# Performance work log

Hardware: AMD Instinct MI355X
Metric: run time of the kernel (lower is better)

Reference implementation:

```python
import jax, jax.numpy as jnp
from jax import lax
import numpy as np

V, B, E, H, T = 32000, 32, 64, 256, 128
START = 0


def setup_inputs() -> dict:
    key = jax.random.key(0)
    ks = jax.random.split(key, 17)
    s = 0.1  # keep logits in a sane range
    inp = {
        "input_x": jax.random.randint(ks[0], (B, T), 0, V, dtype=jnp.int32),
        "emb": jax.random.normal(ks[1], (V, E), jnp.float32) * s,
        "Wi": jax.random.normal(ks[2], (E, H), jnp.float32) * s,
        "Ui": jax.random.normal(ks[3], (H, H), jnp.float32) * s,
        "bi": jax.random.normal(ks[4], (H,), jnp.float32) * s,
        "Wf": jax.random.normal(ks[5], (E, H), jnp.float32) * s,
        "Uf": jax.random.normal(ks[6], (H, H), jnp.float32) * s,
        "bf": jax.random.normal(ks[7], (H,), jnp.float32) * s,
        "Wog": jax.random.normal(ks[8], (E, H), jnp.float32) * s,
        "Uog": jax.random.normal(ks[9], (H, H), jnp.float32) * s,
        "bog": jax.random.normal(ks[10], (H,), jnp.float32) * s,
        "Wc": jax.random.normal(ks[11], (E, H), jnp.float32) * s,
        "Uc": jax.random.normal(ks[12], (H, H), jnp.float32) * s,
        "bc": jax.random.normal(ks[13], (H,), jnp.float32) * s,
        "Wo": jax.random.normal(ks[14], (H, V), jnp.float32) * s,
        "bo": jax.random.normal(ks[15], (V,), jnp.float32) * s,
        "start_token": START,
    }
    return inp


def reference(input_x, emb, Wi, Ui, bi, Wf, Uf, bf, Wog, Uog, bog,
              Wc, Uc, bc, Wo, bo, start_token):
    b, t = input_x.shape
    h_dim = Ui.shape[0]
    # teacher-forcing inputs: [start_emb, emb(x_0..x_{T-2})], time-major [T,B,E]
    x0 = emb[jnp.full((b,), start_token, dtype=jnp.int32)]  # [B,E]
    emb_x = jnp.transpose(emb[input_x], (1, 0, 2))          # [T,B,E]
    xs = jnp.concatenate([x0[None], emb_x[:-1]], axis=0)    # [T,B,E]

    def step(carry, x):
        h, c = carry
        i = jax.nn.sigmoid(x @ Wi + h @ Ui + bi)
        f = jax.nn.sigmoid(x @ Wf + h @ Uf + bf)
        o = jax.nn.sigmoid(x @ Wog + h @ Uog + bog)
        c_bar = jnp.tanh(x @ Wc + h @ Uc + bc)
        c = f * c + i * c_bar
        h = o * jnp.tanh(c)
        logits = h @ Wo + bo                                # [B,V]
        return (h, c), jax.nn.log_softmax(logits, axis=-1)

    h0 = jnp.zeros((b, h_dim), jnp.float32)
    _, logp = lax.scan(step, (h0, h0), xs)                  # [T,B,V]
    logp = jnp.transpose(logp, (1, 0, 2))                   # [B,T,V]
    # -sum over all tokens of log p(target); equals one_hot * log(softmax) sum
    tgt_logp = jnp.take_along_axis(logp, input_x[..., None].astype(jnp.int32), axis=-1)[..., 0]
    return -jnp.sum(tgt_logp)
```

## Files before the change

### kernel.cpp

```cpp
#include <hip/hip_runtime.h>
#include <hip/hip_bf16.h>
#include <math.h>

#define V 32000
#define B 32
#define E 64
#define H 256
#define T 128
#define NROW (B*T)
#define NC 128
#define NVB (V/NC)

typedef __attribute__((ext_vector_type(8))) short bf16x8;
typedef __attribute__((ext_vector_type(4))) float f32x4;
typedef __attribute__((ext_vector_type(8))) unsigned short u16x8;

#define OFF_XS   0
#define OFF_XW   (OFF_XS + NROW*E)
#define OFF_HB   (OFF_XW + NROW*4*H)
#define OFF_PS   (OFF_HB + NROW*H/2)
#define OFF_TL   (OFF_PS + NVB*NROW)
#define OFF_U8   (OFF_TL + NROW)
#define OFF_SC   (OFF_U8 + H*H)
#define OFF_TGT  (OFF_SC + 16)

static __device__ __forceinline__ unsigned short f2bf(float f) {
    union { float f; unsigned int u; } x; x.f = f;
    unsigned int r = x.u + 0x7fffu + ((x.u >> 16) & 1u);
    return (unsigned short)(r >> 16);
}
static __device__ __forceinline__ float bf2f(unsigned short u) {
    union { unsigned int u; float f; } x; x.u = ((unsigned int)u) << 16; return x.f;
}
static __device__ __forceinline__ float sigmoidf_(float x) { return 1.f / (1.f + __expf(-x)); }
static __device__ __forceinline__ float tanhf_(float x)    { return 2.f / (1.f + __expf(-2.f * x)) - 1.f; }

#if defined(__has_builtin)
#if __has_builtin(__builtin_amdgcn_sdot4)
#define HAVE_SDOT4 1
#endif
#if __has_builtin(__builtin_amdgcn_global_load_lds)
#define HAVE_GLL 1
#endif
#endif
static __device__ __forceinline__ int dot4i8(unsigned int a, unsigned int b, int c) {
#ifdef HAVE_SDOT4
    return __builtin_amdgcn_sdot4((int)a, (int)b, c, false);
#else
    c += (int)(char)(a)       * (int)(char)(b);
    c += (int)(char)(a >> 8)  * (int)(char)(b >> 8);
    c += (int)(char)(a >> 16) * (int)(char)(b >> 16);
    c += (int)(char)(a >> 24) * (int)(char)(b >> 24);
    return c;
#endif
}
static __device__ __forceinline__ void stage16(const char* g, char* l, int lane) {
#ifdef HAVE_GLL
    __builtin_amdgcn_global_load_lds(
        (const __attribute__((address_space(1))) void*)g,
        (__attribute__((address_space(3))) void*)l, 16, 0, 0);
    (void)lane;
#else
    *(uint4*)(l + lane * 16) = *(const uint4*)g;
#endif
}

__global__ void lstm_embed(const int* __restrict__ x, const float* __restrict__ emb,
                           const int* __restrict__ start, float* __restrict__ xs,
                           float* __restrict__ out, int* __restrict__ tgtrow) {
    int idx = blockIdx.x * 256 + threadIdx.x;
    if (idx == 0) out[0] = 0.f;
    if (idx < NROW) tgtrow[idx] = x[(idx & 31) * T + (idx >> 5)];
    if (idx >= T * B * E) return;
    int t   = idx / (B * E);
    int rem = idx - t * (B * E);
    int b   = rem >> 6;
    int e   = rem & 63;
    int tok = (t == 0) ? start[0] : x[b * T + (t - 1)];
    xs[idx] = emb[tok * E + e];
}

__global__ __launch_bounds__(256) void lstm_xw(
        const float* __restrict__ xs, unsigned short* __restrict__ xwq,
        const float* __restrict__ Wi, const float* __restrict__ Wf,
        const float* __restrict__ Wog, const float* __restrict__ Wc,
        const float* __restrict__ bi, const float* __restrict__ bf,
        const float* __restrict__ bog, const float* __restrict__ bc) {
    __shared__ float xsl[32][65];
    const int t = blockIdx.x, tid = threadIdx.x;
    for (int i = tid; i < 32 * 64; i += 256) {
        int b = i >> 6, e = i & 63;
        xsl[b][e] = xs[(size_t)(t * 32 + b) * 64 + e];
    }
    __syncthreads();
    const int b = tid & 31, jg = tid >> 5;
    for (int jj = 0; jj < 32; ++jj) {
        const int j = jg * 32 + jj;
        float a0 = bi[j], a1 = bf[j], a2 = bog[j], a3 = bc[j];
        #pragma unroll 8
        for (int e = 0; e < E; ++e) {
            float xe = xsl[b][e];
            a0 += xe * Wi [e * H + j];
            a1 += xe * Wf [e * H + j];
            a2 += xe * Wog[e * H + j];
            a3 += xe * Wc [e * H + j];
        }
        ushort4 v;
        v.x = f2bf(a0); v.y = f2bf(a1); v.z = f2bf(a2); v.w = f2bf(a3);
        *(ushort4*)(xwq + ((size_t)(t * 32 + b) * 256 + j) * 4) = v;
    }
}

__global__ __launch_bounds__(256) void lstm_umax(
        const float* __restrict__ Ui, const float* __restrict__ Uf,
        const float* __restrict__ Uog, const float* __restrict__ Uc,
        float* __restrict__ sc) {
    const int g = blockIdx.x;
    const float* U = (g == 0) ? Ui : (g == 1) ? Uf : (g == 2) ? Uog : Uc;
    float m = 0.f;
    for (int i = threadIdx.x; i < H * H; i += 256) m = fmaxf(m, fabsf(U[i]));
    __shared__ float red[256];
    red[threadIdx.x] = m;
    __syncthreads();
    for (int off = 128; off > 0; off >>= 1) {
        if (threadIdx.x < off) red[threadIdx.x] = fmaxf(red[threadIdx.x], red[threadIdx.x + off]);
        __syncthreads();
    }
    if (threadIdx.x == 0) sc[g] = fmaxf(red[0], 1e-20f);
}

__global__ __launch_bounds__(256) void lstm_uq8(
        const float* __restrict__ Ui, const float* __restrict__ Uf,
        const float* __restrict__ Uog, const float* __restrict__ Uc,
        const float* __restrict__ sc, unsigned int* __restrict__ UQ8) {
    const int idx = blockIdx.x * 256 + threadIdx.x;
    const int k4 = idx >> 8, j = idx & 255;
    float inv[4] = { 127.f / sc[0], 127.f / sc[1], 127.f / sc[2], 127.f / sc[3] };
    const float* Ug[4] = { Ui, Uf, Uog, Uc };
    uint4 out;
    unsigned int* op = (unsigned int*)&out;
    #pragma unroll
    for (int g = 0; g < 4; ++g) {
        unsigned int w = 0;
        #pragma unroll
        for (int kk = 0; kk < 4; ++kk) {
            float v = Ug[g][(size_t)(k4 * 4 + kk) * H + j];
            int q = __float2int_rn(v * inv[g]);
            q = q > 127 ? 127 : (q < -127 ? -127 : q);
            w |= ((unsigned int)(q & 255)) << (kk * 8);
        }
        op[g] = w;
    }
    *(uint4*)(UQ8 + (size_t)idx * 4) = out;
}

__global__ __launch_bounds__(1024) void lstm_recur_i8(
        const unsigned short* __restrict__ xwq, const uint4* __restrict__ UQ8,
        const float* __restrict__ sc, unsigned short* __restrict__ hb) {
    __shared__ unsigned int hq8[2][64];
    __shared__ int4 red[4][256];
    const int b = blockIdx.x, tid = threadIdx.x;
    const int j = tid & 255, q = tid >> 8;
    const float f0 = sc[0] * (1.f / 16129.f), f1 = sc[1] * (1.f / 16129.f);
    const float f2 = sc[2] * (1.f / 16129.f), f3 = sc[3] * (1.f / 16129.f);
    float c_ = 0.f;

    for (int t = 0; t < T; ++t) {
        if (t > 0) {
            const uint4* up = UQ8 + (size_t)(q * 16) * 256 + j;
            const unsigned int* hrow = hq8[t & 1] + q * 16;
            int a0 = 0, a1 = 0, a2 = 0, a3 = 0;
            #pragma unroll
            for (int m = 0; m < 16; ++m) {
                uint4 u = up[(size_t)m * 256];
                unsigned int hv = hrow[m];
                a0 = dot4i8(u.x, hv, a0);
                a1 = dot4i8(u.y, hv, a1);
                a2 = dot4i8(u.z, hv, a2);
                a3 = dot4i8(u.w, hv, a3);
            }
            red[q][j] = make_int4(a0, a1, a2, a3);
        }
        __syncthreads();
        if (tid < 256) {
            ushort4 xw = *(const ushort4*)(xwq + ((size_t)(t * 32 + b) * 256 + j) * 4);
            float pi = bf2f(xw.x), pf = bf2f(xw.y), po = bf2f(xw.z), pc = bf2f(xw.w);
            if (t > 0) {
                int4 r0 = red[0][j], r1 = red[1][j], r2 = red[2][j], r3 = red[3][j];
                pi += (float)(r0.x + r1.x + r2.x + r3.x) * f0;
                pf += (float)(r0.y + r1.y + r2.y + r3.y) * f1;
                po += (float)(r0.z + r1.z + r2.z + r3.z) * f2;
                pc += (float)(r0.w + r1.w + r2.w + r3.w) * f3;
            }
            c_ = sigmoidf_(pf) * c_ + sigmoidf_(pi) * tanhf_(pc);
            float h = sigmoidf_(po) * tanhf_(c_);
            hb[(size_t)(t * B + b) * H + j] = f2bf(h);
            ((char*)hq8[(t + 1) & 1])[j] = (char)__float2int_rn(h * 127.f);
        }
        __syncthreads();
    }
}

__global__ __launch_bounds__(256) void lstm_wot(const float* __restrict__ Wo,
                                                unsigned short* __restrict__ WoT) {
    __shared__ unsigned short tle[64][65];
    const int n0 = blockIdx.x * 64, k0 = blockIdx.y * 64;
    const int tid = threadIdx.x;
    for (int i = tid; i < 64 * 64; i += 256) {
        int kk = i >> 6, nn = i & 63;
        tle[kk][nn] = f2bf(Wo[(size_t)(k0 + kk) * V + n0 + nn]);
    }
    __syncthreads();
    for (int c = tid; c < 512; c += 256) {
        int nn = c >> 3, kc = c & 7;
        u16x8 v;
        #pragma unroll
        for (int e = 0; e < 8; ++e) v[e] = tle[kc * 8 + e][nn];
        *(u16x8*)(WoT + (size_t)(n0 + nn) * H + k0 + kc * 8) = v;
    }
}

__global__ __launch_bounds__(1024, 4) void lstm_logits_mfma(
        const unsigned short* __restrict__ hb, const unsigned short* __restrict__ WoT,
        const float* __restrict__ bo, const int* __restrict__ tgtrow,
        float* __restrict__ ps, float* __restrict__ tl) {
    __shared__ char ab0[65536];
    __shared__ char ab1[65536];
    __shared__ float s_red[4][132];
    const int tid = threadIdx.x, lane = tid & 63, wid = tid >> 6;
    const int wr = wid >> 2, wc = wid & 3;
    const int lr = lane & 15, lg = lane >> 4;
    const int swz = lr & 7;
    const int vb = blockIdx.x * NC;

    #define STAGE_TILE(dst_, srcbase_) { _Pragma("unroll") \
        for (int i_ = 0; i_ < 4; ++i_) { \
            int chunk_ = (wid * 4 + i_) * 64 + lane; \
            int row_ = chunk_ >> 5, c16_ = chunk_ & 31; \
            int srcc_ = c16_ ^ (row_ & 7); \
            stage16((const char*)(srcbase_) + row_ * 512 + srcc_ * 16, \
                    (dst_) + (wid * 4 + i_) * 1024, lane); \
        } }

    STAGE_TILE(ab0, (const char*)(WoT + (size_t)vb * H));
    __syncthreads();
    bf16x8 Bf[2][8];
    {
        const char* bBase = ab0 + (wc * 32 + lr) * 512;
        #pragma unroll
        for (int nf = 0; nf < 2; ++nf)
            #pragma unroll
            for (int ks = 0; ks < 8; ++ks)
                Bf[nf][ks] = *(const bf16x8*)(bBase + nf * 16 * 512 + (((ks * 4 + lg) ^ swz) << 4));
    }
    float bocol[2] = { bo[vb + wc * 32 + lr], bo[vb + wc * 32 + 16 + lr] };
    STAGE_TILE(ab1, (const char*)hb);
    __syncthreads();

    for (int rb = 0; rb < NROW / 128; ++rb) {
        char* curb = (rb & 1) ? ab0 : ab1;
        char* nxtb = (rb & 1) ? ab1 : ab0;
        if (rb + 1 < NROW / 128)
            STAGE_TILE(nxtb, (const char*)(hb + (size_t)(rb + 1) * 128 * H));

        f32x4 acc[2][2] = {};
        const char* aBase = curb + (wr * 32 + lr) * 512;
        #pragma unroll
        for (int ks = 0; ks < 8; ++ks) {
            const int co = ((ks * 4 + lg) ^ swz) << 4;
            bf16x8 a0 = *(const bf16x8*)(aBase + co);
            bf16x8 a1 = *(const bf16x8*)(aBase + 16 * 512 + co);
            acc[0][0] = __builtin_amdgcn_mfma_f32_16x16x32_bf16(a0, Bf[0][ks], acc[0][0], 0, 0, 0);
            acc[0][1] = __builtin_amdgcn_mfma_f32_16x16x32_bf16(a0, Bf[1][ks], acc[0][1], 0, 0, 0);
            acc[1][0] = __builtin_amdgcn_mfma_f32_16x16x32_bf16(a1, Bf[0][ks], acc[1][0], 0, 0, 0);
            acc[1][1] = __builtin_amdgcn_mfma_f32_16x16x32_bf16(a1, Bf[1][ks], acc[1][1], 0, 0, 0);
        }

        const int col0 = vb + wc * 32 + lr, col1 = col0 + 16;
        #pragma unroll
        for (int mf = 0; mf < 2; ++mf)
            #pragma unroll
            for (int r = 0; r < 4; ++r) {
                const int row_l = wr * 32 + mf * 16 + lg * 4 + r;
                float v0 = acc[mf][0][r] + bocol[0];
                float v1 = acc[mf][1][r] + bocol[1];
                const int tg = tgtrow[rb * 128 + row_l];
                if (tg == col0) tl[rb * 128 + row_l] = v0;
                if (tg == col1) tl[rb * 128 + row_l] = v1;
                float e = __expf(v0) + __expf(v1);
                e += __shfl_xor(e, 1); e += __shfl_xor(e, 2);
                e += __shfl_xor(e, 4); e += __shfl_xor(e, 8);
                if (lr == 0) s_red[wc][row_l] = e;
            }
        __syncthreads();
        if (tid < 128)
            ps[(size_t)blockIdx.x * NROW + rb * 128 + tid] =
                s_red[0][tid] + s_red[1][tid] + s_red[2][tid] + s_red[3][tid];
        __syncthreads();
    }
    #undef STAGE_TILE
}

__global__ __launch_bounds__(256) void lstm_lse(
        const float* __restrict__ ps, const float* __restrict__ tl,
        float* __restrict__ out) {
    const int row = blockIdx.x * 256 + threadIdx.x;
    float s = 0.f;
    for (int c = 0; c < NVB; ++c) s += ps[(size_t)c * NROW + row];
    float nll = logf(s) - tl[row];
    __shared__ float red[256];
    red[threadIdx.x] = nll;
    __syncthreads();
    for (int off = 128; off > 0; off >>= 1) {
        if (threadIdx.x < off) red[threadIdx.x] += red[threadIdx.x + off];
        __syncthreads();
    }
    if (threadIdx.x == 0) atomicAdd(out, red[0]);
}

extern "C" void kernel_launch(void* const* d_in, const int* in_sizes, int n_in,
                              void* d_out, int out_size, void* d_ws, size_t ws_size,
                              hipStream_t stream) {
    const int*   x     = (const int*)d_in[0];
    const float* emb   = (const float*)d_in[1];
    const float* Wi    = (const float*)d_in[2];
    const float* Ui    = (const float*)d_in[3];
    const float* bi    = (const float*)d_in[4];
    const float* Wf    = (const float*)d_in[5];
    const float* Uf    = (const float*)d_in[6];
    const float* bf    = (const float*)d_in[7];
    const float* Wog   = (const float*)d_in[8];
    const float* Uog   = (const float*)d_in[9];
    const float* bog   = (const float*)d_in[10];
    const float* Wc    = (const float*)d_in[11];
    const float* Uc    = (const float*)d_in[12];
    const float* bc    = (const float*)d_in[13];
    const float* Wo    = (const float*)d_in[14];
    const float* bo    = (const float*)d_in[15];
    const int*   start = (const int*)d_in[16];
    float* ws  = (float*)d_ws;
    float* out = (float*)d_out;

    float*          xs   = ws + OFF_XS;
    unsigned short* xwq  = (unsigned short*)(ws + OFF_XW);
    unsigned short* WoT  = (unsigned short*)(ws + OFF_XW);
    unsigned short* hbf  = (unsigned short*)(ws + OFF_HB);
    float*          psB  = ws + OFF_PS;
    float*          tlB  = ws + OFF_TL;
    unsigned int*   UQ8  = (unsigned int*)(ws + OFF_U8);
    float*          scB  = ws + OFF_SC;
    int*            tgtr = (int*)(ws + OFF_TGT);

    lstm_embed <<<(T * B * E + 255) / 256, 256, 0, stream>>>(x, emb, start, xs, out, tgtr);
    lstm_xw    <<<T, 256, 0, stream>>>(xs, xwq, Wi, Wf, Wog, Wc, bi, bf, bog, bc);
    lstm_umax  <<<4, 256, 0, stream>>>(Ui, Uf, Uog, Uc, scB);
    lstm_uq8   <<<(H / 4) * H / 256, 256, 0, stream>>>(Ui, Uf, Uog, Uc, scB, UQ8);
    lstm_recur_i8<<<B, 1024, 0, stream>>>(xwq, (const uint4*)UQ8, scB, hbf);
    lstm_wot   <<<dim3(V / 64, H / 64), 256, 0, stream>>>(Wo, WoT);
    lstm_logits_mfma<<<NVB, 1024, 0, stream>>>(hbf, WoT, bo, tgtr, psB, tlB);
    lstm_lse   <<<NROW / 256, 256, 0, stream>>>(psB, tlB, out);
}
```

Baseline: 438.4 us.

## Split logits kernel rows across two blocks with 512-thread blocks

The logits MFMA kernel now launches a 2D grid that splits the 4096 rows into two halves, each block using 512 threads and 64-row tiles, with half-size LDS buffers. The aim is to use more of the GPU's compute units (250 blocks to 500) and to cut LDS per block, which raises occupancy. Target indices are now staged in shared memory once per tile. In exchange, each block keeps its Wo slice in registers while processing only half as many rows, so Wo fragments are loaded twice overall, and the loop runs more iterations, each ending in two barriers.

```diff
diff --git a/kernel.cpp b/kernel.cpp
--- a/kernel.cpp
+++ b/kernel.cpp
@@ -220,20 +220,22 @@
     }
 }
 
-__global__ __launch_bounds__(1024, 4) void lstm_logits_mfma(
+__global__ __launch_bounds__(512, 4) void lstm_logits_mfma(
         const unsigned short* __restrict__ hb, const unsigned short* __restrict__ WoT,
         const float* __restrict__ bo, const int* __restrict__ tgtrow,
         float* __restrict__ ps, float* __restrict__ tl) {
-    __shared__ char ab0[65536];
-    __shared__ char ab1[65536];
-    __shared__ float s_red[4][132];
+    __shared__ char ab0[32768];
+    __shared__ char ab1[32768];
+    __shared__ float s_red[4][72];
+    __shared__ int   tgt_l[64];
     const int tid = threadIdx.x, lane = tid & 63, wid = tid >> 6;
     const int wr = wid >> 2, wc = wid & 3;
     const int lr = lane & 15, lg = lane >> 4;
     const int swz = lr & 7;
     const int vb = blockIdx.x * NC;
-
-    #define STAGE_TILE(dst_, srcbase_) { _Pragma("unroll") \
+    const int rbase = blockIdx.y * (NROW / 2);
+
+    #define STAGE32(dst_, srcbase_) { _Pragma("unroll") \
         for (int i_ = 0; i_ < 4; ++i_) { \
             int chunk_ = (wid * 4 + i_) * 64 + lane; \
             int row_ = chunk_ >> 5, c16_ = chunk_ & 31; \
@@ -242,11 +244,13 @@
                     (dst_) + (wid * 4 + i_) * 1024, lane); \
         } }
 
-    STAGE_TILE(ab0, (const char*)(WoT + (size_t)vb * H));
+    STAGE32(ab0, (const char*)(WoT + (size_t)vb * H));
+    STAGE32(ab1, (const char*)(WoT + (size_t)(vb + 64) * H));
     __syncthreads();
     bf16x8 Bf[2][8];
     {
-        const char* bBase = ab0 + (wc * 32 + lr) * 512;
+        const char* bBase = (wc < 2) ? (ab0 + (wc * 32 + lr) * 512)
+                                     : (ab1 + ((wc - 2) * 32 + lr) * 512);
         #pragma unroll
         for (int nf = 0; nf < 2; ++nf)
             #pragma unroll
@@ -254,14 +258,16 @@
                 Bf[nf][ks] = *(const bf16x8*)(bBase + nf * 16 * 512 + (((ks * 4 + lg) ^ swz) << 4));
     }
     float bocol[2] = { bo[vb + wc * 32 + lr], bo[vb + wc * 32 + 16 + lr] };
-    STAGE_TILE(ab1, (const char*)hb);
-    __syncthreads();
-
-    for (int rb = 0; rb < NROW / 128; ++rb) {
-        char* curb = (rb & 1) ? ab0 : ab1;
-        char* nxtb = (rb & 1) ? ab1 : ab0;
-        if (rb + 1 < NROW / 128)
-            STAGE_TILE(nxtb, (const char*)(hb + (size_t)(rb + 1) * 128 * H));
+    __syncthreads();
+    STAGE32(ab0, (const char*)(hb + (size_t)rbase * H));
+    __syncthreads();
+
+    for (int rb = 0; rb < 32; ++rb) {
+        char* curb = (rb & 1) ? ab1 : ab0;
+        char* nxtb = (rb & 1) ? ab0 : ab1;
+        if (rb + 1 < 32)
+            STAGE32(nxtb, (const char*)(hb + (size_t)(rbase + (rb + 1) * 64) * H));
+        if (tid < 64) tgt_l[tid] = tgtrow[rbase + rb * 64 + tid];
 
         f32x4 acc[2][2] = {};
         const char* aBase = curb + (wr * 32 + lr) * 512;
@@ -284,21 +290,21 @@
                 const int row_l = wr * 32 + mf * 16 + lg * 4 + r;
                 float v0 = acc[mf][0][r] + bocol[0];
                 float v1 = acc[mf][1][r] + bocol[1];
-                const int tg = tgtrow[rb * 128 + row_l];
-                if (tg == col0) tl[rb * 128 + row_l] = v0;
-                if (tg == col1) tl[rb * 128 + row_l] = v1;
+                const int tg = tgt_l[row_l];
+                if (tg == col0) tl[rbase + rb * 64 + row_l] = v0;
+                if (tg == col1) tl[rbase + rb * 64 + row_l] = v1;
                 float e = __expf(v0) + __expf(v1);
                 e += __shfl_xor(e, 1); e += __shfl_xor(e, 2);
                 e += __shfl_xor(e, 4); e += __shfl_xor(e, 8);
                 if (lr == 0) s_red[wc][row_l] = e;
             }
         __syncthreads();
-        if (tid < 128)
-            ps[(size_t)blockIdx.x * NROW + rb * 128 + tid] =
+        if (tid < 64)
+            ps[(size_t)blockIdx.x * NROW + rbase + rb * 64 + tid] =
                 s_red[0][tid] + s_red[1][tid] + s_red[2][tid] + s_red[3][tid];
         __syncthreads();
     }
-    #undef STAGE_TILE
+    #undef STAGE32
 }
 
 __global__ __launch_bounds__(256) void lstm_lse(
@@ -357,6 +363,6 @@
     lstm_uq8   <<<(H / 4) * H / 256, 256, 0, stream>>>(Ui, Uf, Uog, Uc, scB, UQ8);
     lstm_recur_i8<<<B, 1024, 0, stream>>>(xwq, (const uint4*)UQ8, scB, hbf);
     lstm_wot   <<<dim3(V / 64, H / 64), 256, 0, stream>>>(Wo, WoT);
-    lstm_logits_mfma<<<NVB, 1024, 0, stream>>>(hbf, WoT, bo, tgtr, psB, tlB);
+    lstm_logits_mfma<<<dim3(NVB, 2), 512, 0, stream>>>(hbf, WoT, bo, tgtr, psB, tlB);
     lstm_lse   <<<NROW / 256, 256, 0, stream>>>(psB, tlB, out);
 }
```

After: 466.5 us. 6.4% more time.
